# Kernel tuning notes

Hardware: AMD Instinct MI355X
Metric: run time of the kernel (lower is better)

## Reference

```python
import jax, jax.numpy as jnp
import numpy as np

B, N, D, E, H = 2, 384, 768, 64, 512  # batch, nodes, node_dim, edge_dim, hidden_dim
LN_EPS = 1e-5


def _layer_norm(x, g, b):
    mu = jnp.mean(x, axis=-1, keepdims=True)
    var = jnp.mean((x - mu) ** 2, axis=-1, keepdims=True)
    return (x - mu) * jax.lax.rsqrt(var + LN_EPS) * g + b


def setup_inputs() -> dict:
    key = jax.random.key(0)
    ks = jax.random.split(key, 10)
    s = 0.02
    nodes = jax.random.normal(ks[0], (B, N, D), jnp.float32)
    edges = jax.random.normal(ks[1], (B, N, N, E), jnp.float32)
    adjacency = (jax.random.uniform(ks[2], (B, N, N)) < 0.1).astype(jnp.float32)
    # node_update: Linear(D+E -> H), LayerNorm(H), ReLU, Linear(H -> D)
    nw1 = jax.random.normal(ks[3], (D + E, H), jnp.float32) * s
    nb1 = jnp.zeros((H,), jnp.float32)
    ng = jnp.ones((H,), jnp.float32)
    nbt = jnp.zeros((H,), jnp.float32)
    nw2 = jax.random.normal(ks[4], (H, D), jnp.float32) * s
    nb2 = jnp.zeros((D,), jnp.float32)
    # edge_update: Linear(E+2D -> H), LayerNorm(H), ReLU, Linear(H -> E)
    ew1 = jax.random.normal(ks[5], (E + 2 * D, H), jnp.float32) * s
    eb1 = jnp.zeros((H,), jnp.float32)
    eg = jnp.ones((H,), jnp.float32)
    ebt = jnp.zeros((H,), jnp.float32)
    ew2 = jax.random.normal(ks[6], (H, E), jnp.float32) * s
    eb2 = jnp.zeros((E,), jnp.float32)
    return dict(nodes=nodes, edges=edges, adjacency=adjacency,
                nw1=nw1, nb1=nb1, ng=ng, nbt=nbt, nw2=nw2, nb2=nb2,
                ew1=ew1, eb1=eb1, eg=eg, ebt=ebt, ew2=ew2, eb2=eb2)


def reference(nodes, edges, adjacency, nw1, nb1, ng, nbt, nw2, nb2,
              ew1, eb1, eg, ebt, ew2, eb2):
    Bb, Nn, Dd = nodes.shape
    Ee = edges.shape[-1]
    # --- node update ---
    # messages = sum_j cat([edges*adj, nodes_i], -1)
    #          = cat([sum_j edges_adj, N * nodes], -1)  (nodes_expanded is constant over j)
    agg = jnp.einsum('bije,bij->bie', edges, adjacency)          # [B,N,E]
    messages = jnp.concatenate([agg, nodes * Nn], axis=-1)        # [B,N,E+D] -- torch cat order is [edges_adj, nodes]
    # NOTE: torch concat order is [edges_adj, nodes_expanded] -> first E dims are edge agg.
    # Linear weight nw1 laid out as [E+D? ...]: here rows 0:E multiply agg, E:E+D multiply nodes.
    h = _layer_norm(messages @ nw1 + nb1, ng, nbt)                # [B,N,H]
    nodes_updated = nodes + jax.nn.relu(h) @ nw2 + nb2            # [B,N,D]
    # --- edge update ---
    # edge_input = cat([edges, nodes_i, nodes_j], -1); first Linear split to avoid
    # materializing [B,N,N,E+2D].
    We, Wi, Wj = ew1[:Ee], ew1[Ee:Ee + Dd], ew1[Ee + Dd:]
    he = (jnp.einsum('bije,eh->bijh', edges, We)
          + (nodes @ Wi)[:, :, None, :]
          + (nodes @ Wj)[:, None, :, :]
          + eb1)                                                  # [B,N,N,H]
    he = jax.nn.relu(_layer_norm(he, eg, ebt))
    edges_updated = edges + he @ ew2 + eb2                        # [B,N,N,E]
    return nodes_updated, edges_updated
```

## Files before the change

### kernel.cpp

```cpp
#include <hip/hip_runtime.h>

typedef unsigned int u32;
typedef unsigned short u16;

#define Bx 2
#define Nx 384
#define Dx 768
#define Ex 64
#define Hx 512
#define LN_EPS 1e-5f
#define NODES_OUT (Bx * Nx * Dx)
#define MSGW (Ex + Dx)

#define JT2 32
#define NJT (Nx / JT2)

typedef __attribute__((ext_vector_type(8))) short     bf16x8;
typedef __attribute__((ext_vector_type(8))) _Float16  halfx8;
typedef __attribute__((ext_vector_type(4))) float     f32x4;

__device__ int   g_mode;
__device__ float g_Xi[Bx * Nx * Hx];
__device__ float g_Xj[Bx * Nx * Hx];
__device__ __align__(16) u16 g_W1p[32 * 2 * 512];
__device__ __align__(16) u16 g_W2p[4 * 16 * 512];
__device__ __align__(16) u16 g_W1ph[32 * 2 * 512];
__device__ __align__(16) u16 g_W2ph[4 * 16 * 512];
__device__ __align__(16) u16 g_ndh[NODES_OUT];
__device__ __align__(16) u16 g_ndl[NODES_OUT];
__device__ __align__(16) u16 g_msgh[Bx * Nx * MSGW];
__device__ __align__(16) u16 g_msgl[Bx * Nx * MSGW];
#define W1P_SZ (32 * 2 * 512)
#define W2P_SZ (4 * 16 * 512)
#define WIJ_SZ (64 * 24 * 512)
#define NW1_SZ (32 * 26 * 512)
#define NW2_SZ (48 * 16 * 512)
__device__ __align__(16) u16 g_WIJh[WIJ_SZ];
__device__ __align__(16) u16 g_NW1h[NW1_SZ];
__device__ __align__(16) u16 g_NW2h[NW2_SZ];

__device__ __forceinline__ float b2f(u16 u) {
    union { float f; u32 i; } v; v.i = ((u32)u) << 16; return v.f;
}
__device__ __forceinline__ u16 f2b(float f) {
    union { float f; u32 u; } v; v.f = f;
    return (u16)((v.u + 0x7FFFu + ((v.u >> 16) & 1u)) >> 16);
}
__device__ __forceinline__ void tsplit(float v, u16& hi, u16& lo) {
    u32 u = __float_as_uint(v);
    hi = (u16)(u >> 16);
    float r = v - __uint_as_float(u & 0xFFFF0000u);
    lo = (u16)(__float_as_uint(r) >> 16);
}
__device__ __forceinline__ float h2f(u16 h) {
    u32 s = ((u32)(h & 0x8000u)) << 16;
    u32 e = (h >> 10) & 0x1Fu;
    u32 m = h & 0x3FFu;
    union { u32 u; float f; } v;
    if (e == 0) {
        union { u32 u; float f; } a, b;
        a.u = s | 0x38800000u;
        b.u = s | 0x38800000u | (m << 13);
        return b.f - a.f;
    }
    if (e == 31) { v.u = s | 0x7F800000u | (m << 13); return v.f; }
    v.u = s | ((e + 112u) << 23) | (m << 13);
    return v.f;
}
__device__ __forceinline__ u16 f2h(float f) {
    union { float f; u32 u; } v; v.f = f;
    u32 s = (v.u >> 16) & 0x8000u;
    u32 ef = (v.u >> 23) & 0xFFu;
    u32 m = v.u & 0x7FFFFFu;
    if (ef == 0xFFu) return (u16)(s | 0x7C00u | (m ? 0x200u : 0u));
    int e = (int)ef - 127 + 15;
    if (e >= 31) return (u16)(s | 0x7C00u);
    if (e <= 0) {
        if (e < -10) return (u16)s;
        m |= 0x800000u;
        u32 sh = (u32)(14 - e);
        u32 r = (m + (1u << (sh - 1)) - 1u + ((m >> sh) & 1u)) >> sh;
        return (u16)(s | r);
    }
    u32 r = (m + 0xFFFu + ((m >> 13) & 1u)) >> 13;
    return (u16)(s | (((u32)e << 10) + r));
}
__device__ __forceinline__ float ldin(const void* p, size_t i, int m) {
    switch (m) {
        case 0:  return b2f(((const u16*)p)[i]);
        case 1:  return ((const float*)p)[i];
        case 2:  return h2f(((const u16*)p)[i]);
        default: return (float)((const double*)p)[i];
    }
}
__device__ __forceinline__ void stout(void* p, size_t i, float v, int m) {
    switch (m) {
        case 0:  ((u16*)p)[i] = f2b(v); break;
        case 1:  ((float*)p)[i] = v; break;
        case 2:  ((u16*)p)[i] = f2h(v); break;
        default: ((double*)p)[i] = (double)v; break;
    }
}
template<int MODE> __device__ __forceinline__ float uf(u16 v) {
    if constexpr (MODE == 0) return b2f(v); else return h2f(v);
}
template<int MODE> __device__ __forceinline__ u16 fu(float f) {
    if constexpr (MODE == 0) return f2b(f); else return f2h(f);
}
template<int MODE>
__device__ __forceinline__ f32x4 mm16(bf16x8 a, bf16x8 b, f32x4 c) {
    if constexpr (MODE == 0) {
        return __builtin_amdgcn_mfma_f32_16x16x32_bf16(a, b, c, 0, 0, 0);
    } else {
        union { bf16x8 s; halfx8 h; } ua, ub;
        ua.s = a; ub.s = b;
        return __builtin_amdgcn_mfma_f32_16x16x32_f16(ua.h, ub.h, c, 0, 0, 0);
    }
}

__global__ void k_mode(const u16* __restrict__ ng) {
    u16 a = ng[0], b = ng[1], d3 = ng[3];
    int m;
    if (a == 0x3F80u) m = 0;
    else if (a == 0x3C00u) m = 2;
    else if (a == 0u && b == 0x3F80u) m = 1;
    else if (a == 0u && d3 == 0x3FF0u) m = 3;
    else m = 2;
    g_mode = m;
}

__global__ __launch_bounds__(512) void k_pack(const void* __restrict__ ew1,
                                              const void* __restrict__ ew2) {
    int m = g_mode;
    if (m != 0 && m != 2) return;
    const u16* w1 = (const u16*)ew1;
    const u16* w2 = (const u16*)ew2;
    int t = blockIdx.x * 512 + threadIdx.x;
    {
        int tl = t >> 10, ks = (t >> 9) & 1, l = (t >> 3) & 63, i = t & 7;
        int e = ks * 32 + ((l >> 4) << 3) + i;
        int h = (tl << 4) + (l & 15);
        g_W1p[t] = w1[(size_t)e * Hx + h];
    }
    {
        int en = t >> 13, ks = (t >> 9) & 15, l = (t >> 3) & 63, i = t & 7;
        int k = ks * 32 + ((l >> 4) << 3) + i;
        int e = (en << 4) + (l & 15);
        g_W2p[t] = w2[(size_t)k * Ex + e];
    }
}

__global__ __launch_bounds__(512) void k_pack_all_f32(const float* __restrict__ ew1,
                                                      const float* __restrict__ ew2,
                                                      const float* __restrict__ nw1,
                                                      const float* __restrict__ nw2) {
    if (g_mode != 1) return;
    const int total = W1P_SZ + W2P_SZ + WIJ_SZ + NW1_SZ + NW2_SZ;
    for (int t = blockIdx.x * 512 + threadIdx.x; t < total; t += gridDim.x * 512) {
        if (t < W1P_SZ) {
            int tl = t >> 10, ks = (t >> 9) & 1, l = (t >> 3) & 63, i = t & 7;
            int e = ks * 32 + ((l >> 4) << 3) + i;
            int h = (tl << 4) + (l & 15);
            g_W1ph[t] = f2b(ew1[(size_t)e * Hx + h]);
        } else if (t < W1P_SZ + W2P_SZ) {
            int u = t - W1P_SZ;
            int en = u >> 13, ks = (u >> 9) & 15, l = (u >> 3) & 63, i = u & 7;
            int k = ks * 32 + ((l >> 4) << 3) + i;
            int e = (en << 4) + (l & 15);
            g_W2ph[u] = f2b(ew2[(size_t)k * Ex + e]);
        } else if (t < W1P_SZ + W2P_SZ + WIJ_SZ) {
            int u = t - W1P_SZ - W2P_SZ;
            int i = u & 7, l = (u >> 3) & 63, rest = u >> 9;
            int ks = rest % 24, tile = rest / 24;
            int k = ks * 32 + ((l >> 4) << 3) + i;
            int col = (tile << 4) + (l & 15);
            float v = (col < Hx) ? ew1[(size_t)(Ex + k) * Hx + col]
                                 : ew1[(size_t)(Ex + Dx + k) * Hx + (col - Hx)];
            g_WIJh[u] = f2b(v);
        } else if (t < W1P_SZ + W2P_SZ + WIJ_SZ + NW1_SZ) {
            int u = t - W1P_SZ - W2P_SZ - WIJ_SZ;
            int i = u & 7, l = (u >> 3) & 63, rest = u >> 9;
            int ks = rest % 26, tile = rest / 26;
            int k = ks * 32 + ((l >> 4) << 3) + i;
            int col = (tile << 4) + (l & 15);
            g_NW1h[u] = f2b(nw1[(size_t)k * Hx + col]);
        } else {
            int u = t - W1P_SZ - W2P_SZ - WIJ_SZ - NW1_SZ;
            int i = u & 7, l = (u >> 3) & 63, rest = u >> 9;
            int ks = rest & 15, tile = rest >> 4;
            int k = (ks << 5) + ((l >> 4) << 3) + i;
            int col = (tile << 4) + (l & 15);
            g_NW2h[u] = f2b(nw2[(size_t)k * Dx + col]);
        }
    }
}

__global__ __launch_bounds__(512) void k_agg(const float* __restrict__ edges,
                                             const float* __restrict__ adj,
                                             const float* __restrict__ nodes) {
    if (g_mode != 1) return;
    int t = threadIdx.x, bi = blockIdx.x;
    __shared__ float sarr[512];
    {
        int e = t & 63, jg = t >> 6;
        const float* eb = edges + (size_t)bi * Nx * Ex;
        const float* ab = adj + (size_t)bi * Nx;
        float acc = 0.f;
        for (int j = jg * 48; j < jg * 48 + 48; ++j)
            acc += eb[(size_t)j * Ex + e] * ab[j];
        sarr[t] = acc;
    }
    __syncthreads();
    if (t < Ex) {
        float s = 0.f;
        #pragma unroll
        for (int g = 0; g < 8; ++g) s += sarr[g * 64 + t];
        tsplit(s, g_msgh[(size_t)bi * MSGW + t], g_msgl[(size_t)bi * MSGW + t]);
    }
    for (int d = t; d < Dx; d += 512) {
        float v = nodes[(size_t)bi * Dx + d] * (float)Nx;
        tsplit(v, g_msgh[(size_t)bi * MSGW + Ex + d], g_msgl[(size_t)bi * MSGW + Ex + d]);
    }
    for (int i = bi * 512 + t; i < NODES_OUT; i += Bx * Nx * 512) {
        tsplit(nodes[i], g_ndh[i], g_ndl[i]);
    }
}

__global__ __launch_bounds__(512) void k_xixj(const void* __restrict__ nodes,
                                              const void* __restrict__ ew1,
                                              const void* __restrict__ eb1) {
    int m = g_mode;
    if (m == 1) return;
    int t = threadIdx.x;
    int bi = blockIdx.x;
    __shared__ float nd[Dx];
    for (int d = t; d < Dx; d += 512) nd[d] = ldin(nodes, (size_t)bi * Dx + d, m);
    __syncthreads();

    float ai = ldin(eb1, t, m);
    float aj = 0.f;
    for (int d = 0; d < Dx; ++d) {
        float nv = nd[d];
        ai += nv * ldin(ew1, (size_t)(Ex + d) * Hx + t, m);
        aj += nv * ldin(ew1, (size_t)(Ex + Dx + d) * Hx + t, m);
    }
    g_Xi[(size_t)bi * Hx + t] = ai;
    g_Xj[(size_t)bi * Hx + t] = aj;
}

__global__ __launch_bounds__(512) void k_xixj_f32(const float* __restrict__ eb1) {
    if (g_mode != 1) return;
    int t = threadIdx.x, w = t >> 6, l = t & 63, lg = l >> 4, li = l & 15;
    int blk = blockIdx.x;
    int ch = blk & 1;
    int half = (blk >> 1) & 1;
    int r0 = (blk >> 2) << 4;

    f32x4 acc[2] = {};
    const u16* Ah = g_ndh + (size_t)(r0 + li) * Dx;
    const u16* Al = g_ndl + (size_t)(r0 + li) * Dx;
    for (int ks = 0; ks < 24; ++ks) {
        bf16x8 ah = *(const bf16x8*)(Ah + ks * 32 + (lg << 3));
        bf16x8 al = *(const bf16x8*)(Al + ks * 32 + (lg << 3));
        #pragma unroll
        for (int tt = 0; tt < 2; ++tt) {
            int tile = half * 32 + ch * 16 + (w << 1) + tt;
            bf16x8 bh = *(const bf16x8*)(g_WIJh + ((tile * 24 + ks) << 9) + (l << 3));
            acc[tt] = mm16<0>(ah, bh, acc[tt]);
            acc[tt] = mm16<0>(al, bh, acc[tt]);
        }
    }
    float* dst = half ? g_Xj : g_Xi;
    #pragma unroll
    for (int tt = 0; tt < 2; ++tt) {
        int col = ((ch * 16 + (w << 1) + tt) << 4) + li;
        float bias = half ? 0.f : eb1[col];
        #pragma unroll
        for (int r = 0; r < 4; ++r) {
            int row = r0 + (lg << 2) + r;
            dst[(size_t)row * Hx + col] = acc[tt][r] + bias;
        }
    }
}

__global__ __launch_bounds__(512) void k_node(const void* __restrict__ nodes,
                                              const void* __restrict__ edges,
                                              const void* __restrict__ adj,
                                              const void* __restrict__ nw1,
                                              const void* __restrict__ nb1,
                                              const void* __restrict__ ng,
                                              const void* __restrict__ nbt,
                                              const void* __restrict__ nw2,
                                              const void* __restrict__ nb2,
                                              void* __restrict__ d_out) {
    int m = g_mode;
    if (m == 1) return;
    int t = threadIdx.x;
    int bi = blockIdx.x;
    __shared__ float msg[Ex + Dx];
    __shared__ float p[Hx];
    __shared__ float sarr[Hx], qarr[Hx];

    {
        int e = t & 63, jg = t >> 6;
        float acc = 0.f;
        for (int j = jg * 48; j < jg * 48 + 48; ++j)
            acc += ldin(edges, (size_t)bi * Nx * Ex + (size_t)j * Ex + e, m)
                 * ldin(adj, (size_t)bi * Nx + j, m);
        sarr[t] = acc;
    }
    for (int d = t; d < Dx; d += 512)
        msg[Ex + d] = ldin(nodes, (size_t)bi * Dx + d, m) * (float)Nx;
    __syncthreads();
    if (t < Ex) {
        float s = 0.f;
        for (int g = 0; g < 8; ++g) s += sarr[g * 64 + t];
        msg[t] = s;
    }
    __syncthreads();

    float h = ldin(nb1, t, m);
    for (int k = 0; k < Ex + Dx; ++k)
        h += msg[k] * ldin(nw1, (size_t)k * Hx + t, m);

    sarr[t] = h; qarr[t] = h * h;
    __syncthreads();
    for (int s = 256; s > 0; s >>= 1) {
        if (t < s) { sarr[t] += sarr[t + s]; qarr[t] += qarr[t + s]; }
        __syncthreads();
    }
    float mu  = sarr[0] * (1.f / Hx);
    float var = qarr[0] * (1.f / Hx) - mu * mu;
    float rv  = rsqrtf(var + LN_EPS);
    p[t] = fmaxf((h - mu) * rv * ldin(ng, t, m) + ldin(nbt, t, m), 0.f);
    __syncthreads();

    float o0 = ldin(nodes, (size_t)bi * Dx + t, m) + ldin(nb2, t, m);
    float o1 = 0.f;
    if (t < Dx - Hx)
        o1 = ldin(nodes, (size_t)bi * Dx + Hx + t, m) + ldin(nb2, Hx + t, m);
    for (int hh = 0; hh < Hx; ++hh) {
        float pv = p[hh];
        o0 += pv * ldin(nw2, (size_t)hh * Dx + t, m);
        if (t < Dx - Hx) o1 += pv * ldin(nw2, (size_t)hh * Dx + Hx + t, m);
    }
    stout(d_out, (size_t)bi * Dx + t, o0, m);
    if (t < Dx - Hx) stout(d_out, (size_t)bi * Dx + Hx + t, o1, m);
}

__global__ __launch_bounds__(512) void k_node_f32(const float* __restrict__ nodes,
                                                  const float* __restrict__ nb1,
                                                  const float* __restrict__ ng,
                                                  const float* __restrict__ nbt,
                                                  const float* __restrict__ nb2,
                                                  float* __restrict__ out) {
    if (g_mode != 1) return;
    int t = threadIdx.x, w = t >> 6, l = t & 63, lg = l >> 4, li = l & 15;
    int r0 = blockIdx.x * 16;

    __shared__ __align__(16) u16 P[16 * Hx];
    __shared__ float lnS[8][16];
    __shared__ float lnQ[8][16];

    f32x4 acc[4] = {};
    const u16* Ah = g_msgh + (size_t)(r0 + li) * MSGW;
    const u16* Al = g_msgl + (size_t)(r0 + li) * MSGW;
    for (int ks = 0; ks < 26; ++ks) {
        bf16x8 ah = *(const bf16x8*)(Ah + ks * 32 + (lg << 3));
        bf16x8 al = *(const bf16x8*)(Al + ks * 32 + (lg << 3));
        #pragma unroll
        for (int tt = 0; tt < 4; ++tt) {
            int tile = (w << 2) + tt;
            bf16x8 bh = *(const bf16x8*)(g_NW1h + ((tile * 26 + ks) << 9) + (l << 3));
            acc[tt] = mm16<0>(ah, bh, acc[tt]);
            acc[tt] = mm16<0>(al, bh, acc[tt]);
        }
    }
    #pragma unroll
    for (int tt = 0; tt < 4; ++tt) {
        float bias = nb1[(((w << 2) + tt) << 4) + li];
        #pragma unroll
        for (int r = 0; r < 4; ++r) acc[tt][r] += bias;
    }

    float s0[4] = {0.f, 0.f, 0.f, 0.f}, q0[4] = {0.f, 0.f, 0.f, 0.f};
    #pragma unroll
    for (int tt = 0; tt < 4; ++tt) {
        #pragma unroll
        for (int r = 0; r < 4; ++r) {
            float v = acc[tt][r];
            s0[r] += v; q0[r] += v * v;
        }
    }
    #pragma unroll
    for (int msk = 1; msk < 16; msk <<= 1) {
        #pragma unroll
        for (int r = 0; r < 4; ++r) {
            s0[r] += __shfl_xor(s0[r], msk);
            q0[r] += __shfl_xor(q0[r], msk);
        }
    }
    if (li == 0) {
        #pragma unroll
        for (int r = 0; r < 4; ++r) {
            lnS[w][(lg << 2) + r] = s0[r];
            lnQ[w][(lg << 2) + r] = q0[r];
        }
    }
    __syncthreads();
    float mu[4], rv[4];
    #pragma unroll
    for (int r = 0; r < 4; ++r) {
        int jl = (lg << 2) + r;
        float S = 0.f, Q = 0.f;
        #pragma unroll
        for (int ww = 0; ww < 8; ++ww) { S += lnS[ww][jl]; Q += lnQ[ww][jl]; }
        float m_ = S * (1.f / Hx);
        float v_ = Q * (1.f / Hx) - m_ * m_;
        mu[r] = m_;
        rv[r] = rsqrtf(v_ + LN_EPS);
    }

    #pragma unroll
    for (int tt = 0; tt < 4; ++tt) {
        int col = (((w << 2) + tt) << 4) + li;
        float gm = ng[col];
        float bt = nbt[col];
        #pragma unroll
        for (int r = 0; r < 4; ++r) {
            int jl = (lg << 2) + r;
            float pv = fmaxf((acc[tt][r] - mu[r]) * rv[r] * gm + bt, 0.f);
            P[(jl << 9) + (col ^ ((jl & 7) << 3))] = f2b(pv);
        }
    }
    __syncthreads();

    f32x4 o[6] = {};
    int jr = li;
    int rswz = (jr & 7) << 3;
    for (int ks = 0; ks < 16; ++ks) {
        bf16x8 pa = *(const bf16x8*)(P + (jr << 9) + (((ks << 5) + (lg << 3)) ^ rswz));
        #pragma unroll
        for (int tt = 0; tt < 6; ++tt) {
            int tile = w * 6 + tt;
            bf16x8 bh = *(const bf16x8*)(g_NW2h + ((tile * 16 + ks) << 9) + (l << 3));
            o[tt] = mm16<0>(pa, bh, o[tt]);
        }
    }
    #pragma unroll
    for (int tt = 0; tt < 6; ++tt) {
        int col = ((w * 6 + tt) << 4) + li;
        float b2v = nb2[col];
        #pragma unroll
        for (int r = 0; r < 4; ++r) {
            int row = r0 + (lg << 2) + r;
            out[(size_t)row * Dx + col] = nodes[(size_t)row * Dx + col] + b2v + o[tt][r];
        }
    }
}

#define JT 8
__global__ __launch_bounds__(512) void k_edge(const void* __restrict__ edges,
                                              const void* __restrict__ ew1,
                                              const void* __restrict__ eg,
                                              const void* __restrict__ ebt,
                                              const void* __restrict__ ew2,
                                              const void* __restrict__ eb2,
                                              void* __restrict__ d_out) {
    int m = g_mode;
    if (m != 3) return;
    int t = threadIdx.x;
    int blk = blockIdx.x;
    int jt4 = blk % NJT;
    int bi = blk / NJT;
    int b  = bi / Nx;

    __shared__ float Ej[JT][Ex];
    __shared__ float p[JT][Hx];
    __shared__ float sarr[512], qarr[512];
    __shared__ float mus[JT], rvs[JT];

    for (int sub = 0; sub < 4; ++sub) {
        int j0 = jt4 * 32 + sub * 8;
        size_t ebase = ((size_t)bi * Nx + j0) * Ex;

        { int jj = t >> 6, e = t & 63;
          Ej[jj][e] = ldin(edges, ebase + (size_t)jj * Ex + e, m); }

        float xi = g_Xi[(size_t)bi * Hx + t];
        float acc[JT];
        #pragma unroll
        for (int jj = 0; jj < JT; ++jj)
            acc[jj] = xi + g_Xj[((size_t)b * Nx + j0 + jj) * Hx + t];
        __syncthreads();

        for (int e = 0; e < Ex; ++e) {
            float w = ldin(ew1, (size_t)e * Hx + t, m);
            #pragma unroll
            for (int jj = 0; jj < JT; ++jj)
                acc[jj] += Ej[jj][e] * w;
        }
        #pragma unroll
        for (int jj = 0; jj < JT; ++jj) p[jj][t] = acc[jj];
        __syncthreads();

        {
            int g = t >> 6, l = t & 63;
            float s = 0.f, q = 0.f;
            for (int k = 0; k < 8; ++k) {
                float v = p[g][l + 64 * k];
                s += v; q += v * v;
            }
            sarr[t] = s; qarr[t] = q;
            __syncthreads();
            for (int st = 32; st > 0; st >>= 1) {
                if (l < st) { sarr[t] += sarr[t + st]; qarr[t] += qarr[t + st]; }
                __syncthreads();
            }
            if (l == 0) {
                float mu  = sarr[t] * (1.f / Hx);
                float var = qarr[t] * (1.f / Hx) - mu * mu;
                mus[g] = mu;
                rvs[g] = rsqrtf(var + LN_EPS);
            }
        }
        __syncthreads();

        float gm = ldin(eg, t, m), bt2 = ldin(ebt, t, m);
        #pragma unroll
        for (int jj = 0; jj < JT; ++jj)
            p[jj][t] = fmaxf((acc[jj] - mus[jj]) * rvs[jj] * gm + bt2, 0.f);
        __syncthreads();

        {
            int jj = t >> 6, e = t & 63;
            float o = Ej[jj][e] + ldin(eb2, e, m);
            for (int hh = 0; hh < Hx; ++hh)
                o += p[jj][hh] * ldin(ew2, (size_t)hh * Ex + e, m);
            stout(d_out, (size_t)NODES_OUT + ebase + (size_t)jj * Ex + e, o, m);
        }
        __syncthreads();
    }
}

template<int MODE>
__global__ __launch_bounds__(512) void k_edge_mfma(const void* __restrict__ edges,
                                                   const void* __restrict__ eg,
                                                   const void* __restrict__ ebt,
                                                   const void* __restrict__ eb2,
                                                   void* __restrict__ d_out) {
    if (g_mode != MODE) return;
    const u16* E16 = (const u16*)edges;
    int t  = threadIdx.x;
    int w  = t >> 6, l = t & 63;
    int lg = l >> 4, li = l & 15;
    int blk = blockIdx.x;
    int jt = blk % NJT;
    int bi = blk / NJT;
    int b  = bi / Nx;
    int j0 = jt * JT2;

    __shared__ __align__(16) u16 P[JT2 * Hx];
    __shared__ float lnS[4][JT2];
    __shared__ float lnQ[4][JT2];

    int jm = w >> 2;
    int nw = w & 3;

    bf16x8 a0, a1;
    {
        const u16* src = E16 + ((size_t)bi * Nx + j0 + jm * 16 + li) * Ex + (lg << 3);
        a0 = *(const bf16x8*)src;
        a1 = *(const bf16x8*)(src + 32);
    }
    f32x4 acc[8];
    #pragma unroll
    for (int tt = 0; tt < 8; ++tt) {
        int tg = nw * 8 + tt;
        bf16x8 b0 = *(const bf16x8*)(g_W1p + ((tg * 2 + 0) << 9) + (l << 3));
        bf16x8 b1 = *(const bf16x8*)(g_W1p + ((tg * 2 + 1) << 9) + (l << 3));
        f32x4 c = {0.f, 0.f, 0.f, 0.f};
        c = mm16<MODE>(a0, b0, c);
        c = mm16<MODE>(a1, b1, c);
        acc[tt] = c;
    }
    #pragma unroll
    for (int tt = 0; tt < 8; ++tt) {
        int h = ((nw * 8 + tt) << 4) + li;
        float xi = g_Xi[(size_t)bi * Hx + h];
        #pragma unroll
        for (int r = 0; r < 4; ++r) {
            int jl = jm * 16 + lg * 4 + r;
            acc[tt][r] += xi + g_Xj[((size_t)b * Nx + j0 + jl) * Hx + h];
        }
    }

    float s0[4] = {0.f, 0.f, 0.f, 0.f}, q0[4] = {0.f, 0.f, 0.f, 0.f};
    #pragma unroll
    for (int tt = 0; tt < 8; ++tt) {
        #pragma unroll
        for (int r = 0; r < 4; ++r) {
            float v = acc[tt][r];
            s0[r] += v; q0[r] += v * v;
        }
    }
    #pragma unroll
    for (int msk = 1; msk < 16; msk <<= 1) {
        #pragma unroll
        for (int r = 0; r < 4; ++r) {
            s0[r] += __shfl_xor(s0[r], msk);
            q0[r] += __shfl_xor(q0[r], msk);
        }
    }
    if (li == 0) {
        #pragma unroll
        for (int r = 0; r < 4; ++r) {
            lnS[nw][jm * 16 + lg * 4 + r] = s0[r];
            lnQ[nw][jm * 16 + lg * 4 + r] = q0[r];
        }
    }
    __syncthreads();
    float mu[4], rv[4];
    #pragma unroll
    for (int r = 0; r < 4; ++r) {
        int jl = jm * 16 + lg * 4 + r;
        float S = lnS[0][jl] + lnS[1][jl] + lnS[2][jl] + lnS[3][jl];
        float Q = lnQ[0][jl] + lnQ[1][jl] + lnQ[2][jl] + lnQ[3][jl];
        float m_ = S * (1.f / Hx);
        float v_ = Q * (1.f / Hx) - m_ * m_;
        mu[r] = m_;
        rv[r] = rsqrtf(v_ + LN_EPS);
    }

    const u16* g16  = (const u16*)eg;
    const u16* bt16 = (const u16*)ebt;
    #pragma unroll
    for (int tt = 0; tt < 8; ++tt) {
        int h = ((nw * 8 + tt) << 4) + li;
        float gm = uf<MODE>(g16[h]);
        float bt = uf<MODE>(bt16[h]);
        #pragma unroll
        for (int r = 0; r < 4; ++r) {
            int jl = jm * 16 + lg * 4 + r;
            float pv = fmaxf((acc[tt][r] - mu[r]) * rv[r] * gm + bt, 0.f);
            P[(jl << 9) + (h ^ ((jl & 7) << 3))] = fu<MODE>(pv);
        }
    }
    __syncthreads();

    f32x4 o = {0.f, 0.f, 0.f, 0.f};
    int jr = jm * 16 + li;
    int rswz = (jr & 7) << 3;
    #pragma unroll
    for (int ks = 0; ks < 16; ++ks) {
        bf16x8 a  = *(const bf16x8*)(P + (jr << 9) + ((ks * 32 + (lg << 3)) ^ rswz));
        bf16x8 bb = *(const bf16x8*)(g_W2p + ((nw * 16 + ks) << 9) + (l << 3));
        o = mm16<MODE>(a, bb, o);
    }
    int e = (nw << 4) + li;
    float e2 = uf<MODE>(((const u16*)eb2)[e]);
    u16* OUT = (u16*)d_out + NODES_OUT;
    #pragma unroll
    for (int r = 0; r < 4; ++r) {
        int jl = jm * 16 + lg * 4 + r;
        size_t gi = ((size_t)bi * Nx + j0 + jl) * Ex + e;
        float ev = uf<MODE>(E16[gi]);
        OUT[gi] = fu<MODE>(ev + e2 + o[r]);
    }
}

__global__ __launch_bounds__(512, 8) void k_edge_f32(const float* __restrict__ edges,
                                                     const float* __restrict__ eg,
                                                     const float* __restrict__ ebt,
                                                     const float* __restrict__ eb2,
                                                     float* __restrict__ out) {
    if (g_mode != 1) return;
    int t = threadIdx.x;
    int w = t >> 6, l = t & 63;
    int lg = l >> 4, li = l & 15;
    int blk = blockIdx.x;
    int jt = blk % NJT;
    int bi = blk / NJT;
    int b  = bi / Nx;
    int j0 = jt * JT2;

    __shared__ __align__(16) u16 Eh[JT2 * Ex];
    __shared__ __align__(16) u16 El[JT2 * Ex];
    __shared__ __align__(16) u16 P [JT2 * Hx];
    __shared__ float lnS[4][JT2];
    __shared__ float lnQ[4][JT2];

    int jm = w >> 2, nw = w & 3;

    #pragma unroll
    for (int it = 0; it < 4; ++it) {
        int idx = t + it * 512;
        int row = idx >> 6, k = idx & 63;
        float v = edges[((size_t)bi * Nx + j0 + row) * Ex + k];
        int sl = (row << 6) + (k ^ ((row & 7) << 3));
        tsplit(v, Eh[sl], El[sl]);
    }
    __syncthreads();

    bf16x8 ah0, al0, ah1, al1;
    {
        int r_ = jm * 16 + li;
        int base = r_ << 6;
        int sw = (r_ & 7) << 3;
        int k0 = (lg << 3) ^ sw;
        int k1 = ((lg << 3) + 32) ^ sw;
        ah0 = *(const bf16x8*)(Eh + base + k0);
        al0 = *(const bf16x8*)(El + base + k0);
        ah1 = *(const bf16x8*)(Eh + base + k1);
        al1 = *(const bf16x8*)(El + base + k1);
    }

    f32x4 acc[8];
    #pragma unroll
    for (int tt = 0; tt < 8; ++tt) {
        int tg = nw * 8 + tt;
        bf16x8 bh0 = *(const bf16x8*)(g_W1ph + (((tg << 1) + 0) << 9) + (l << 3));
        bf16x8 bh1 = *(const bf16x8*)(g_W1ph + (((tg << 1) + 1) << 9) + (l << 3));
        f32x4 c = {0.f, 0.f, 0.f, 0.f};
        c = mm16<0>(ah0, bh0, c);
        c = mm16<0>(al0, bh0, c);
        c = mm16<0>(ah1, bh1, c);
        c = mm16<0>(al1, bh1, c);
        acc[tt] = c;
    }
    #pragma unroll
    for (int tt = 0; tt < 8; ++tt) {
        int h = ((nw * 8 + tt) << 4) + li;
        float xi = g_Xi[(size_t)bi * Hx + h];
        #pragma unroll
        for (int r = 0; r < 4; ++r) {
            int jl = jm * 16 + lg * 4 + r;
            acc[tt][r] += xi + g_Xj[((size_t)b * Nx + j0 + jl) * Hx + h];
        }
    }

    float s0[4] = {0.f, 0.f, 0.f, 0.f}, q0[4] = {0.f, 0.f, 0.f, 0.f};
    #pragma unroll
    for (int tt = 0; tt < 8; ++tt) {
        #pragma unroll
        for (int r = 0; r < 4; ++r) {
            float v = acc[tt][r];
            s0[r] += v; q0[r] += v * v;
        }
    }
    #pragma unroll
    for (int msk = 1; msk < 16; msk <<= 1) {
        #pragma unroll
        for (int r = 0; r < 4; ++r) {
            s0[r] += __shfl_xor(s0[r], msk);
            q0[r] += __shfl_xor(q0[r], msk);
        }
    }
    if (li == 0) {
        #pragma unroll
        for (int r = 0; r < 4; ++r) {
            lnS[nw][jm * 16 + lg * 4 + r] = s0[r];
            lnQ[nw][jm * 16 + lg * 4 + r] = q0[r];
        }
    }
    __syncthreads();
    float mu[4], rv[4];
    #pragma unroll
    for (int r = 0; r < 4; ++r) {
        int jl = jm * 16 + lg * 4 + r;
        float S = lnS[0][jl] + lnS[1][jl] + lnS[2][jl] + lnS[3][jl];
        float Q = lnQ[0][jl] + lnQ[1][jl] + lnQ[2][jl] + lnQ[3][jl];
        float m_ = S * (1.f / Hx);
        float v_ = Q * (1.f / Hx) - m_ * m_;
        mu[r] = m_;
        rv[r] = rsqrtf(v_ + LN_EPS);
    }

    #pragma unroll
    for (int tt = 0; tt < 8; ++tt) {
        int h = ((nw * 8 + tt) << 4) + li;
        float gm = eg[h];
        float bt = ebt[h];
        #pragma unroll
        for (int r = 0; r < 4; ++r) {
            int jl = jm * 16 + lg * 4 + r;
            float pv = fmaxf((acc[tt][r] - mu[r]) * rv[r] * gm + bt, 0.f);
            P[(jl << 9) + (h ^ ((jl & 7) << 3))] = f2b(pv);
        }
    }
    __syncthreads();

    f32x4 o = {0.f, 0.f, 0.f, 0.f};
    int jr = jm * 16 + li;
    int rswz = (jr & 7) << 3;
    #pragma unroll
    for (int ks = 0; ks < 16; ++ks) {
        bf16x8 pa = *(const bf16x8*)(P + (jr << 9) + (((ks << 5) + (lg << 3)) ^ rswz));
        bf16x8 wh = *(const bf16x8*)(g_W2ph + (((nw << 4) + ks) << 9) + (l << 3));
        o = mm16<0>(pa, wh, o);
    }
    int e = (nw << 4) + li;
    float e2 = eb2[e];
    float* OUT = out + NODES_OUT;
    #pragma unroll
    for (int r = 0; r < 4; ++r) {
        int jl = jm * 16 + lg * 4 + r;
        size_t gi = ((size_t)bi * Nx + j0 + jl) * Ex + e;
        OUT[gi] = edges[gi] + e2 + o[r];
    }
}

extern "C" void kernel_launch(void* const* d_in, const int* in_sizes, int n_in,
                              void* d_out, int out_size, void* d_ws, size_t ws_size,
                              hipStream_t stream) {
    const void* nodes = d_in[0];
    const void* edges = d_in[1];
    const void* adj   = d_in[2];
    const void* nw1   = d_in[3];
    const void* nb1   = d_in[4];
    const void* ng    = d_in[5];
    const void* nbt   = d_in[6];
    const void* nw2   = d_in[7];
    const void* nb2   = d_in[8];
    const void* ew1   = d_in[9];
    const void* eb1   = d_in[10];
    const void* eg    = d_in[11];
    const void* ebt   = d_in[12];
    const void* ew2   = d_in[13];
    const void* eb2   = d_in[14];

    k_mode<<<1, 1, 0, stream>>>((const u16*)ng);
    k_pack<<<64, 512, 0, stream>>>(ew1, ew2);
    k_pack_all_f32<<<512, 512, 0, stream>>>((const float*)ew1, (const float*)ew2,
                                            (const float*)nw1, (const float*)nw2);
    k_agg<<<Bx * Nx, 512, 0, stream>>>((const float*)edges, (const float*)adj,
                                       (const float*)nodes);
    k_xixj<<<Bx * Nx, 512, 0, stream>>>(nodes, ew1, eb1);
    k_node<<<Bx * Nx, 512, 0, stream>>>(nodes, edges, adj, nw1, nb1, ng, nbt,
                                        nw2, nb2, d_out);
    k_xixj_f32<<<192, 512, 0, stream>>>((const float*)eb1);
    k_node_f32<<<48, 512, 0, stream>>>((const float*)nodes, (const float*)nb1,
                                       (const float*)ng, (const float*)nbt,
                                       (const float*)nb2, (float*)d_out);
    k_edge<<<Bx * Nx * NJT, 512, 0, stream>>>(edges, ew1, eg, ebt,
                                              ew2, eb2, d_out);
    k_edge_mfma<0><<<Bx * Nx * NJT, 512, 0, stream>>>(edges, eg, ebt, eb2, d_out);
    k_edge_mfma<2><<<Bx * Nx * NJT, 512, 0, stream>>>(edges, eg, ebt, eb2, d_out);
    k_edge_f32<<<Bx * Nx * NJT, 512, 0, stream>>>((const float*)edges,
                                                  (const float*)eg,
                                                  (const float*)ebt,
                                                  (const float*)eb2,
                                                  (float*)d_out);
}
```

Before: 444.1 us.

## Skip dtype-mismatched launches, fold weight packing into agg, reorder edge MFMA

The host reads the input byte size to infer the dtype and launches only the kernels for that dtype, instead of launching every variant and having each early-exit on a device flag. The fp32 weight-packing pass is folded into the aggregation kernel, which drops one launch. In the fp32 edge kernel, the Xi/Xj bias loads now come before the MFMAs and seed the accumulators, the K loop is restructured, and launch bounds drop from 8 to 4 waves per SIMD. This cuts launch and idle-kernel overhead; the reordering may hide load latency but could raise register pressure, and the enlarged shared P buffer (now JT2*Ex*8, the same size as JT2*Hx) is a no-op.

```diff
diff --git a/kernel.cpp b/kernel.cpp
--- a/kernel.cpp
+++ b/kernel.cpp
@@ -11,6 +11,7 @@
 #define LN_EPS 1e-5f
 #define NODES_OUT (Bx * Nx * Dx)
 #define MSGW (Ex + Dx)
+#define NODE_ELEMS (Bx * Nx * Dx)
 
 #define JT2 32
 #define NJT (Nx / JT2)
@@ -150,54 +151,55 @@
     }
 }
 
-__global__ __launch_bounds__(512) void k_pack_all_f32(const float* __restrict__ ew1,
-                                                      const float* __restrict__ ew2,
-                                                      const float* __restrict__ nw1,
-                                                      const float* __restrict__ nw2) {
-    if (g_mode != 1) return;
-    const int total = W1P_SZ + W2P_SZ + WIJ_SZ + NW1_SZ + NW2_SZ;
-    for (int t = blockIdx.x * 512 + threadIdx.x; t < total; t += gridDim.x * 512) {
-        if (t < W1P_SZ) {
-            int tl = t >> 10, ks = (t >> 9) & 1, l = (t >> 3) & 63, i = t & 7;
-            int e = ks * 32 + ((l >> 4) << 3) + i;
-            int h = (tl << 4) + (l & 15);
-            g_W1ph[t] = f2b(ew1[(size_t)e * Hx + h]);
-        } else if (t < W1P_SZ + W2P_SZ) {
-            int u = t - W1P_SZ;
-            int en = u >> 13, ks = (u >> 9) & 15, l = (u >> 3) & 63, i = u & 7;
-            int k = ks * 32 + ((l >> 4) << 3) + i;
-            int e = (en << 4) + (l & 15);
-            g_W2ph[u] = f2b(ew2[(size_t)k * Ex + e]);
-        } else if (t < W1P_SZ + W2P_SZ + WIJ_SZ) {
-            int u = t - W1P_SZ - W2P_SZ;
-            int i = u & 7, l = (u >> 3) & 63, rest = u >> 9;
-            int ks = rest % 24, tile = rest / 24;
-            int k = ks * 32 + ((l >> 4) << 3) + i;
-            int col = (tile << 4) + (l & 15);
-            float v = (col < Hx) ? ew1[(size_t)(Ex + k) * Hx + col]
-                                 : ew1[(size_t)(Ex + Dx + k) * Hx + (col - Hx)];
-            g_WIJh[u] = f2b(v);
-        } else if (t < W1P_SZ + W2P_SZ + WIJ_SZ + NW1_SZ) {
-            int u = t - W1P_SZ - W2P_SZ - WIJ_SZ;
-            int i = u & 7, l = (u >> 3) & 63, rest = u >> 9;
-            int ks = rest % 26, tile = rest / 26;
-            int k = ks * 32 + ((l >> 4) << 3) + i;
-            int col = (tile << 4) + (l & 15);
-            g_NW1h[u] = f2b(nw1[(size_t)k * Hx + col]);
-        } else {
-            int u = t - W1P_SZ - W2P_SZ - WIJ_SZ - NW1_SZ;
-            int i = u & 7, l = (u >> 3) & 63, rest = u >> 9;
-            int ks = rest & 15, tile = rest >> 4;
-            int k = (ks << 5) + ((l >> 4) << 3) + i;
-            int col = (tile << 4) + (l & 15);
-            g_NW2h[u] = f2b(nw2[(size_t)k * Dx + col]);
-        }
+__device__ __forceinline__ void pack_one_f32(int t,
+                                             const float* __restrict__ ew1,
+                                             const float* __restrict__ ew2,
+                                             const float* __restrict__ nw1,
+                                             const float* __restrict__ nw2) {
+    if (t < W1P_SZ) {
+        int tl = t >> 10, ks = (t >> 9) & 1, l = (t >> 3) & 63, i = t & 7;
+        int e = ks * 32 + ((l >> 4) << 3) + i;
+        int h = (tl << 4) + (l & 15);
+        g_W1ph[t] = f2b(ew1[(size_t)e * Hx + h]);
+    } else if (t < W1P_SZ + W2P_SZ) {
+        int u = t - W1P_SZ;
+        int en = u >> 13, ks = (u >> 9) & 15, l = (u >> 3) & 63, i = u & 7;
+        int k = ks * 32 + ((l >> 4) << 3) + i;
+        int e = (en << 4) + (l & 15);
+        g_W2ph[u] = f2b(ew2[(size_t)k * Ex + e]);
+    } else if (t < W1P_SZ + W2P_SZ + WIJ_SZ) {
+        int u = t - W1P_SZ - W2P_SZ;
+        int i = u & 7, l = (u >> 3) & 63, rest = u >> 9;
+        int ks = rest % 24, tile = rest / 24;
+        int k = ks * 32 + ((l >> 4) << 3) + i;
+        int col = (tile << 4) + (l & 15);
+        float v = (col < Hx) ? ew1[(size_t)(Ex + k) * Hx + col]
+                             : ew1[(size_t)(Ex + Dx + k) * Hx + (col - Hx)];
+        g_WIJh[u] = f2b(v);
+    } else if (t < W1P_SZ + W2P_SZ + WIJ_SZ + NW1_SZ) {
+        int u = t - W1P_SZ - W2P_SZ - WIJ_SZ;
+        int i = u & 7, l = (u >> 3) & 63, rest = u >> 9;
+        int ks = rest % 26, tile = rest / 26;
+        int k = ks * 32 + ((l >> 4) << 3) + i;
+        int col = (tile << 4) + (l & 15);
+        g_NW1h[u] = f2b(nw1[(size_t)k * Hx + col]);
+    } else {
+        int u = t - W1P_SZ - W2P_SZ - WIJ_SZ - NW1_SZ;
+        int i = u & 7, l = (u >> 3) & 63, rest = u >> 9;
+        int ks = rest & 15, tile = rest >> 4;
+        int k = (ks << 5) + ((l >> 4) << 3) + i;
+        int col = (tile << 4) + (l & 15);
+        g_NW2h[u] = f2b(nw2[(size_t)k * Dx + col]);
     }
 }
 
 __global__ __launch_bounds__(512) void k_agg(const float* __restrict__ edges,
                                              const float* __restrict__ adj,
-                                             const float* __restrict__ nodes) {
+                                             const float* __restrict__ nodes,
+                                             const float* __restrict__ ew1,
+                                             const float* __restrict__ ew2,
+                                             const float* __restrict__ nw1,
+                                             const float* __restrict__ nw2) {
     if (g_mode != 1) return;
     int t = threadIdx.x, bi = blockIdx.x;
     __shared__ float sarr[512];
@@ -223,6 +225,10 @@
     }
     for (int i = bi * 512 + t; i < NODES_OUT; i += Bx * Nx * 512) {
         tsplit(nodes[i], g_ndh[i], g_ndl[i]);
+    }
+    const int total = W1P_SZ + W2P_SZ + WIJ_SZ + NW1_SZ + NW2_SZ;
+    for (int i = bi * 512 + t; i < total; i += Bx * Nx * 512) {
+        pack_one_f32(i, ew1, ew2, nw1, nw2);
     }
 }
 
@@ -669,7 +675,7 @@
     }
 }
 
-__global__ __launch_bounds__(512, 8) void k_edge_f32(const float* __restrict__ edges,
+__global__ __launch_bounds__(512, 4) void k_edge_f32(const float* __restrict__ edges,
                                                      const float* __restrict__ eg,
                                                      const float* __restrict__ ebt,
                                                      const float* __restrict__ eb2,
@@ -686,7 +692,7 @@
 
     __shared__ __align__(16) u16 Eh[JT2 * Ex];
     __shared__ __align__(16) u16 El[JT2 * Ex];
-    __shared__ __align__(16) u16 P [JT2 * Hx];
+    __shared__ __align__(16) u16 P [JT2 * Ex * 8];
     __shared__ float lnS[4][JT2];
     __shared__ float lnQ[4][JT2];
 
@@ -700,42 +706,36 @@
         int sl = (row << 6) + (k ^ ((row & 7) << 3));
         tsplit(v, Eh[sl], El[sl]);
     }
-    __syncthreads();
-
-    bf16x8 ah0, al0, ah1, al1;
+
+    f32x4 acc[8];
+    #pragma unroll
+    for (int tt = 0; tt < 8; ++tt) {
+        int h = ((nw * 8 + tt) << 4) + li;
+        float xi = g_Xi[(size_t)bi * Hx + h];
+        #pragma unroll
+        for (int r = 0; r < 4; ++r) {
+            int jl = jm * 16 + lg * 4 + r;
+            acc[tt][r] = xi + g_Xj[((size_t)b * Nx + j0 + jl) * Hx + h];
+        }
+    }
+    __syncthreads();
+
     {
         int r_ = jm * 16 + li;
         int base = r_ << 6;
         int sw = (r_ & 7) << 3;
-        int k0 = (lg << 3) ^ sw;
-        int k1 = ((lg << 3) + 32) ^ sw;
-        ah0 = *(const bf16x8*)(Eh + base + k0);
-        al0 = *(const bf16x8*)(El + base + k0);
-        ah1 = *(const bf16x8*)(Eh + base + k1);
-        al1 = *(const bf16x8*)(El + base + k1);
-    }
-
-    f32x4 acc[8];
-    #pragma unroll
-    for (int tt = 0; tt < 8; ++tt) {
-        int tg = nw * 8 + tt;
-        bf16x8 bh0 = *(const bf16x8*)(g_W1ph + (((tg << 1) + 0) << 9) + (l << 3));
-        bf16x8 bh1 = *(const bf16x8*)(g_W1ph + (((tg << 1) + 1) << 9) + (l << 3));
-        f32x4 c = {0.f, 0.f, 0.f, 0.f};
-        c = mm16<0>(ah0, bh0, c);
-        c = mm16<0>(al0, bh0, c);
-        c = mm16<0>(ah1, bh1, c);
-        c = mm16<0>(al1, bh1, c);
-        acc[tt] = c;
-    }
-    #pragma unroll
-    for (int tt = 0; tt < 8; ++tt) {
-        int h = ((nw * 8 + tt) << 4) + li;
-        float xi = g_Xi[(size_t)bi * Hx + h];
-        #pragma unroll
-        for (int r = 0; r < 4; ++r) {
-            int jl = jm * 16 + lg * 4 + r;
-            acc[tt][r] += xi + g_Xj[((size_t)b * Nx + j0 + jl) * Hx + h];
+        #pragma unroll
+        for (int kh = 0; kh < 2; ++kh) {
+            int kk = ((lg << 3) + kh * 32) ^ sw;
+            bf16x8 ah = *(const bf16x8*)(Eh + base + kk);
+            bf16x8 al = *(const bf16x8*)(El + base + kk);
+            #pragma unroll
+            for (int tt = 0; tt < 8; ++tt) {
+                int tg = nw * 8 + tt;
+                bf16x8 bh = *(const bf16x8*)(g_W1ph + (((tg << 1) + kh) << 9) + (l << 3));
+                acc[tt] = mm16<0>(al, bh, acc[tt]);
+                acc[tt] = mm16<0>(ah, bh, acc[tt]);
+            }
         }
     }
 
@@ -829,26 +829,48 @@
     const void* ew2   = d_in[13];
     const void* eb2   = d_in[14];
 
+    int dsz = 0;
+    if (in_sizes && n_in > 0) {
+        if (in_sizes[0] == NODE_ELEMS * 2) dsz = 2;
+        else if (in_sizes[0] == NODE_ELEMS * 4) dsz = 4;
+        else if (in_sizes[0] == NODE_ELEMS * 8) dsz = 8;
+    }
+    bool known  = (dsz != 0);
+    bool do_f32 = (!known) || dsz == 4;
+    bool do_u16 = (!known) || dsz == 2;
+    bool do_f64 = (!known) || dsz == 8;
+
     k_mode<<<1, 1, 0, stream>>>((const u16*)ng);
-    k_pack<<<64, 512, 0, stream>>>(ew1, ew2);
-    k_pack_all_f32<<<512, 512, 0, stream>>>((const float*)ew1, (const float*)ew2,
-                                            (const float*)nw1, (const float*)nw2);
-    k_agg<<<Bx * Nx, 512, 0, stream>>>((const float*)edges, (const float*)adj,
-                                       (const float*)nodes);
-    k_xixj<<<Bx * Nx, 512, 0, stream>>>(nodes, ew1, eb1);
-    k_node<<<Bx * Nx, 512, 0, stream>>>(nodes, edges, adj, nw1, nb1, ng, nbt,
-                                        nw2, nb2, d_out);
-    k_xixj_f32<<<192, 512, 0, stream>>>((const float*)eb1);
-    k_node_f32<<<48, 512, 0, stream>>>((const float*)nodes, (const float*)nb1,
-                                       (const float*)ng, (const float*)nbt,
-                                       (const float*)nb2, (float*)d_out);
-    k_edge<<<Bx * Nx * NJT, 512, 0, stream>>>(edges, ew1, eg, ebt,
-                                              ew2, eb2, d_out);
-    k_edge_mfma<0><<<Bx * Nx * NJT, 512, 0, stream>>>(edges, eg, ebt, eb2, d_out);
-    k_edge_mfma<2><<<Bx * Nx * NJT, 512, 0, stream>>>(edges, eg, ebt, eb2, d_out);
-    k_edge_f32<<<Bx * Nx * NJT, 512, 0, stream>>>((const float*)edges,
-                                                  (const float*)eg,
-                                                  (const float*)ebt,
-                                                  (const float*)eb2,
-                                                  (float*)d_out);
-}
+
+    if (do_u16)
+        k_pack<<<64, 512, 0, stream>>>(ew1, ew2);
+    if (do_f32)
+        k_agg<<<Bx * Nx, 512, 0, stream>>>((const float*)edges, (const float*)adj,
+                                           (const float*)nodes, (const float*)ew1,
+                                           (const float*)ew2, (const float*)nw1,
+                                           (const float*)nw2);
+    if (do_u16 || do_f64) {
+        k_xixj<<<Bx * Nx, 512, 0, stream>>>(nodes, ew1, eb1);
+        k_node<<<Bx * Nx, 512, 0, stream>>>(nodes, edges, adj, nw1, nb1, ng, nbt,
+                                            nw2, nb2, d_out);
+    }
+    if (do_f32) {
+        k_xixj_f32<<<192, 512, 0, stream>>>((const float*)eb1);
+        k_node_f32<<<48, 512, 0, stream>>>((const float*)nodes, (const float*)nb1,
+                                           (const float*)ng, (const float*)nbt,
+                                           (const float*)nb2, (float*)d_out);
+    }
+    if (do_f64)
+        k_edge<<<Bx * Nx * NJT, 512, 0, stream>>>(edges, ew1, eg, ebt,
+                                                  ew2, eb2, d_out);
+    if (do_u16) {
+        k_edge_mfma<0><<<Bx * Nx * NJT, 512, 0, stream>>>(edges, eg, ebt, eb2, d_out);
+        k_edge_mfma<2><<<Bx * Nx * NJT, 512, 0, stream>>>(edges, eg, ebt, eb2, d_out);
+    }
+    if (do_f32)
+        k_edge_f32<<<Bx * Nx * NJT, 512, 0, stream>>>((const float*)edges,
+                                                      (const float*)eg,
+                                                      (const float*)ebt,
+                                                      (const float*)eb2,
+                                                      (float*)d_out);
+}
```

Result: faster. 393.9 us (-11.3%).
